# Performance work log

Measured on AMD Instinct MI355X. Metric: run time of the kernel, lower is better.

## Reference

```python
import jax, jax.numpy as jnp
import numpy as np

B, C, H, W = 16, 256, 96, 96
CQ = C // 8      # 32, query/key channels in CrossAttention
CM = C // 2      # 128, inter_planes


def conv1x1(x, w, b=None):
    # x: [B,Cin,H,W], w: [Cout,Cin]
    y = jnp.einsum('bchw,oc->bohw', x, w)
    if b is not None:
        y = y + b[None, :, None, None]
    return y


def cross_attention(x, wq, bq, wk, bk, wv, bv, gamma):
    # criss-cross (axial H and W) attention with -inf diagonal on the H branch
    b_, c_, h_, w_ = x.shape
    q = conv1x1(x, wq, bq)  # [B,CQ,H,W]
    k = conv1x1(x, wk, bk)
    v = conv1x1(x, wv, bv)  # [B,C,H,W]
    # energy over column (H axis): [B,H,W,H], masked diag h==h'
    e_h = jnp.einsum('bchw,bckw->bhwk', q, k)
    diag = jnp.eye(h_, dtype=bool)[None, :, None, :]  # [1,H,1,H]
    e_h = jnp.where(diag, -jnp.inf, e_h)
    # energy over row (W axis): [B,H,W,W]
    e_w = jnp.einsum('bchw,bchv->bhwv', q, k)
    att = jax.nn.softmax(jnp.concatenate([e_h, e_w], axis=3), axis=3)
    a_h, a_w = att[..., :h_], att[..., h_:]
    out_h = jnp.einsum('bckw,bhwk->bchw', v, a_h)
    out_w = jnp.einsum('bchv,bhwv->bchw', v, a_w)
    return gamma * (out_h + out_w) + x


def spatial_weighted(x, w_q_right, w_v_right, w_up, b_up):
    b_, _, h_, w_ = x.shape
    inp = conv1x1(x, w_v_right).reshape(b_, CM, h_ * w_)        # [B,CM,HW]
    mask = conv1x1(x, w_q_right).reshape(b_, 1, h_ * w_)        # [B,1,HW]
    mask = jax.nn.softmax(mask, axis=2)
    ctx = jnp.einsum('bcn,bon->bco', inp, mask)                 # [B,CM,1]
    ctx = jnp.einsum('bci,oc->boi', ctx, w_up) + b_up[None, :, None]  # [B,C,1]
    mask_ch = jax.nn.sigmoid(ctx)[..., None]                    # [B,C,1,1]
    return x * mask_ch


def channel_weighted(x, w_q_left, w_v_left):
    b_, _, h_, w_ = x.shape
    g = conv1x1(x, w_q_left)                                    # [B,CM,H,W]
    avg = jnp.mean(g, axis=(2, 3))                              # [B,CM]
    theta = conv1x1(x, w_v_left).reshape(b_, CM, h_ * w_)       # [B,CM,HW]
    ctx = jnp.einsum('bc,bcn->bn', avg, theta)                  # [B,HW]
    ctx = jax.nn.softmax(ctx, axis=1).reshape(b_, 1, h_, w_)
    return x * jax.nn.sigmoid(ctx)


def setup_inputs() -> dict:
    key = jax.random.key(0)
    ks = jax.random.split(key, 16)
    s = lambda fan_in: (2.0 / fan_in) ** 0.5
    inp = {
        'x': jax.random.normal(ks[0], (B, C, H, W), jnp.float32),
        'w_q_right': jax.random.normal(ks[1], (1, C), jnp.float32) * s(C),
        'w_v_right': jax.random.normal(ks[2], (CM, C), jnp.float32) * s(C),
        'w_up': jax.random.normal(ks[3], (C, CM), jnp.float32) * s(CM),
        'b_up': jnp.zeros((C,), jnp.float32),
        'w_q_left': jax.random.normal(ks[4], (CM, C), jnp.float32) * s(C),
        'w_v_left': jax.random.normal(ks[5], (CM, C), jnp.float32) * s(C),
        'cr_wq': jax.random.normal(ks[6], (CQ, C), jnp.float32) * s(C),
        'cr_bq': jnp.zeros((CQ,), jnp.float32),
        'cr_wk': jax.random.normal(ks[7], (CQ, C), jnp.float32) * s(C),
        'cr_bk': jnp.zeros((CQ,), jnp.float32),
        'cr_wv': jax.random.normal(ks[8], (C, C), jnp.float32) * s(C),
        'cr_bv': jnp.zeros((C,), jnp.float32),
        'gamma': jax.random.normal(ks[9], (1,), jnp.float32) * 0.1,
    }
    return inp


def reference(x, w_q_right, w_v_right, w_up, b_up, w_q_left, w_v_left,
              cr_wq, cr_bq, cr_wk, cr_bk, cr_wv, cr_bv, gamma):
    cross = lambda t: cross_attention(t, cr_wq, cr_bq, cr_wk, cr_bk, cr_wv, cr_bv, gamma)
    ctx_channel = cross(spatial_weighted(x, w_q_right, w_v_right, w_up, b_up))
    ctx_spatial = cross(channel_weighted(x, w_q_left, w_v_left))
    return cross(ctx_spatial + ctx_channel)
```

## Files before the change

### kernel.cpp

```cpp
#include <hip/hip_runtime.h>
#include <math.h>

#define Bn 16
#define Cn 256
#define CQn 32
#define CMn 128
#define Hn 96
#define Wn 96
#define Nn 9216
#define PIXn 147456

typedef short bf8 __attribute__((ext_vector_type(8)));
typedef float f32x4 __attribute__((ext_vector_type(4)));
#define MFMA(a,b,c) __builtin_amdgcn_mfma_f32_16x16x32_bf16(a,b,c,0,0,0)

typedef unsigned short ushort_t;

__device__ inline ushort_t f2bf(float f){
  union{float f; unsigned int u;} v; v.f=f;
  unsigned int r = v.u + 0x7fffu + ((v.u>>16)&1u);
  return (ushort_t)(r>>16);
}
__device__ inline float bf2f(ushort_t s){
  union{unsigned int u; float f;} v; v.u = ((unsigned int)s)<<16;
  return v.f;
}

__device__ inline float waveSum(float v){
#pragma unroll
  for(int o=32;o;o>>=1) v += __shfl_down(v,o,64);
  return v;
}
__device__ inline float waveMax(float v){
#pragma unroll
  for(int o=32;o;o>>=1) v = fmaxf(v,__shfl_down(v,o,64));
  return v;
}


__global__ __launch_bounds__(1024) void k_pass1(const float* __restrict__ x,
    const float* __restrict__ wqr, float* __restrict__ xmean,
    float* __restrict__ partp){
  int cg = blockIdx.x, b = blockIdx.y, tid = threadIdx.x;
  __shared__ float r16[16];
  float mp[9];
#pragma unroll
  for(int k=0;k<9;k++) mp[k]=0.f;
  for(int cc=0;cc<16;cc++){
    int c = cg*16+cc;
    const float* row = x + ((size_t)b*Cn + c)*Nn;
    float w = wqr[c];
    float s = 0.f;
#pragma unroll
    for(int k=0;k<9;k++){
      float v = row[k*1024+tid];
      s += v;
      mp[k] += w*v;
    }
    s = waveSum(s);
    if((tid&63)==0) r16[tid>>6]=s;
    __syncthreads();
    if(tid==0){
      float t=0.f;
      for(int i=0;i<16;i++) t+=r16[i];
      xmean[(size_t)b*Cn + c] = t*(1.f/Nn);
    }
    __syncthreads();
  }
  float* dst = partp + ((size_t)cg*Bn + b)*Nn;
#pragma unroll
  for(int k=0;k<9;k++) dst[k*1024+tid]=mp[k];
}

__global__ __launch_bounds__(1024) void k_pass2(const float* __restrict__ x,
    const float* __restrict__ wvec, const float* __restrict__ maskb,
    float* __restrict__ xw, float* __restrict__ partp){
  int cg = blockIdx.x, b = blockIdx.y, tid = threadIdx.x;
  __shared__ float r16[16];
  float cp[9], mk[9];
#pragma unroll
  for(int k=0;k<9;k++){
    cp[k]=0.f;
    mk[k]=maskb[(size_t)b*Nn + k*1024+tid];
  }
  for(int cc=0;cc<16;cc++){
    int c = cg*16+cc;
    const float* row = x + ((size_t)b*Cn + c)*Nn;
    float w = wvec[(size_t)b*Cn + c];
    float s = 0.f;
#pragma unroll
    for(int k=0;k<9;k++){
      float v = row[k*1024+tid];
      s += mk[k]*v;
      cp[k] += w*v;
    }
    s = waveSum(s);
    if((tid&63)==0) r16[tid>>6]=s;
    __syncthreads();
    if(tid==0){
      float t=0.f;
      for(int i=0;i<16;i++) t+=r16[i];
      xw[(size_t)b*Cn + c] = t;
    }
    __syncthreads();
  }
  float* dst = partp + ((size_t)cg*Bn + b)*Nn;
#pragma unroll
  for(int k=0;k<9;k++) dst[k*1024+tid]=cp[k];
}

__global__ void k_red16(const float* __restrict__ part, float* __restrict__ out){
  size_t p = (size_t)blockIdx.x*256 + threadIdx.x;
  float s=0.f;
#pragma unroll
  for(int cg=0;cg<16;cg++) s += part[(size_t)cg*Bn*Nn + p];
  out[p]=s;
}

__global__ void k_small1(const float* __restrict__ xmean, const float* __restrict__ wql,
                         const float* __restrict__ wvl, float* __restrict__ wvec){
  int b=blockIdx.x, t=threadIdx.x;
  __shared__ float xm[Cn];
  __shared__ float av[CMn];
  xm[t] = xmean[b*Cn+t];
  __syncthreads();
  if(t<CMn){
    float s=0.f;
    for(int c=0;c<Cn;c++) s += wql[t*Cn+c]*xm[c];
    av[t]=s;
  }
  __syncthreads();
  float s=0.f;
  for(int m=0;m<CMn;m++) s += av[m]*wvl[m*Cn+t];
  wvec[b*Cn+t]=s;
}

__global__ void k_softmax_n(const float* __restrict__ in, float* __restrict__ out, int mode){
  int b=blockIdx.x, tid=threadIdx.x, lane=tid&63, wid=tid>>6;
  const float* p = in + (size_t)b*Nn;
  __shared__ float red[16];
  __shared__ float bc2[2];
  float mx=-3e38f;
  for(int i=tid;i<Nn;i+=1024) mx=fmaxf(mx,p[i]);
  mx = waveMax(mx);
  if(lane==0) red[wid]=mx;
  __syncthreads();
  if(tid==0){ float m=red[0]; for(int i=1;i<16;i++) m=fmaxf(m,red[i]); bc2[0]=m; }
  __syncthreads();
  mx=bc2[0];
  float s=0.f;
  for(int i=tid;i<Nn;i+=1024) s+=expf(p[i]-mx);
  s = waveSum(s);
  __syncthreads();
  if(lane==0) red[wid]=s;
  __syncthreads();
  if(tid==0){ float t=0.f; for(int i=0;i<16;i++) t+=red[i]; bc2[1]=t; }
  __syncthreads();
  float inv=1.f/bc2[1];
  for(int i=tid;i<Nn;i+=1024){
    float e=expf(p[i]-mx)*inv;
    out[(size_t)b*Nn+i] = mode ? 1.f/(1.f+expf(-e)) : e;
  }
}

__global__ void k_small2(const float* __restrict__ xw, const float* __restrict__ wvr,
                         const float* __restrict__ wup, const float* __restrict__ bup,
                         float* __restrict__ g1){
  int b=blockIdx.x, t=threadIdx.x;
  __shared__ float xs[Cn];
  __shared__ float cx[CMn];
  xs[t]=xw[b*Cn+t];
  __syncthreads();
  if(t<CMn){
    float s=0.f;
    for(int c=0;c<Cn;c++) s += wvr[t*Cn+c]*xs[c];
    cx[t]=s;
  }
  __syncthreads();
  float s=bup[t];
  for(int m=0;m<CMn;m++) s += wup[t*CMn+m]*cx[m];
  g1[b*Cn+t]=1.f/(1.f+expf(-s));
}

__global__ void k_gates(const float* __restrict__ x, const float* __restrict__ g1,
                        const float* __restrict__ m2, ushort_t* __restrict__ t1,
                        ushort_t* __restrict__ t2){
  size_t i4 = ((size_t)blockIdx.x*256 + threadIdx.x)*4;
  int n  = (int)(i4 % Nn);
  int bc = (int)(i4 / Nn);
  int b  = bc / Cn;
  float4 xv = *(const float4*)&x[i4];
  float g = g1[bc];
  float4 mv = *(const float4*)&m2[(size_t)b*Nn + n];
  uint2 a, c;
  a.x = (unsigned)f2bf(xv.x*g) | ((unsigned)f2bf(xv.y*g)<<16);
  a.y = (unsigned)f2bf(xv.z*g) | ((unsigned)f2bf(xv.w*g)<<16);
  c.x = (unsigned)f2bf(xv.x*mv.x) | ((unsigned)f2bf(xv.y*mv.y)<<16);
  c.y = (unsigned)f2bf(xv.z*mv.z) | ((unsigned)f2bf(xv.w*mv.w)<<16);
  *(uint2*)&t1[i4] = a;
  *(uint2*)&t2[i4] = c;
}


__global__ void k_packb(const float* __restrict__ wq, const float* __restrict__ bq,
                        const float* __restrict__ wk, const float* __restrict__ bk,
                        const float* __restrict__ wv, const float* __restrict__ bv,
                        ushort_t* __restrict__ Wp, float* __restrict__ bp){
  int o = blockIdx.x, t = threadIdx.x;
  const float* src; float bs;
  if(o<32){ src = wq + o*Cn; bs = bq[o]; }
  else if(o<64){ src = wk + (o-32)*Cn; bs = bk[o-32]; }
  else { src = wv + (o-64)*Cn; bs = bv[o-64]; }
  Wp[o*Cn+t] = f2bf(src[t]);
  if(t==0) bp[o] = bs;
}

#define AP 40
#define BP 264

__global__ __launch_bounds__(256) void k_gemm_qkv(const ushort_t* __restrict__ x,
    const ushort_t* __restrict__ Wp, const float* __restrict__ bp,
    ushort_t* __restrict__ Yqk, ushort_t* __restrict__ Vb){
  __shared__ ushort_t Ws[320*AP];
  __shared__ ushort_t Bt[64*BP];
  int b  = blockIdx.y;
  int n0 = blockIdx.x*64;
  int tid = threadIdx.x, lane = tid&63, wid = tid>>6;

  {
    const ushort_t* xb = x + (size_t)b*Cn*Nn + n0 + (tid&63);
    int cg = (tid>>6)*8;
#pragma unroll
    for(int p=0;p<8;p++){
      int c8 = p*32 + cg;
      unsigned e0=xb[(size_t)(c8+0)*Nn], e1=xb[(size_t)(c8+1)*Nn];
      unsigned e2=xb[(size_t)(c8+2)*Nn], e3=xb[(size_t)(c8+3)*Nn];
      unsigned e4=xb[(size_t)(c8+4)*Nn], e5=xb[(size_t)(c8+5)*Nn];
      unsigned e6=xb[(size_t)(c8+6)*Nn], e7=xb[(size_t)(c8+7)*Nn];
      uint4 pk;
      pk.x = e0 | (e1<<16); pk.y = e2 | (e3<<16);
      pk.z = e4 | (e5<<16); pk.w = e6 | (e7<<16);
      *(uint4*)&Bt[(tid&63)*BP + c8] = pk;
    }
  }

  f32x4 acc[5][4];
#pragma unroll
  for(int f=0;f<5;f++)
#pragma unroll
    for(int g=0;g<4;g++) acc[f][g] = (f32x4){0.f,0.f,0.f,0.f};

  for(int ki=0;ki<8;ki++){
    __syncthreads();
#pragma unroll
    for(int q=0;q<5;q++){
      int fidx = q*256 + tid;
      int o = fidx>>2, kk = (fidx&3)*8;
      uint4 wv = *(const uint4*)&Wp[o*Cn + ki*32 + kk];
      *(uint4*)&Ws[o*AP + kk] = wv;
    }
    __syncthreads();
    bf8 bfr[4];
#pragma unroll
    for(int g=0;g<4;g++)
      bfr[g] = *(const bf8*)&Bt[(g*16 + (lane&15))*BP + ki*32 + (lane>>4)*8];
#pragma unroll
    for(int f=0;f<5;f++){
      bf8 a = *(const bf8*)&Ws[(wid*80 + f*16 + (lane&15))*AP + (lane>>4)*8];
#pragma unroll
      for(int g=0;g<4;g++) acc[f][g] = MFMA(a, bfr[g], acc[f][g]);
    }
  }

#pragma unroll
  for(int f=0;f<5;f++){
    int ob = wid*80 + f*16 + (lane>>4)*4;
#pragma unroll
    for(int i=0;i<4;i++){
      int o = ob + i;
      float bias = bp[o];
      ushort_t* dst = (o<64) ? (Yqk + ((size_t)b*64 + o)*Nn)
                             : (Vb + ((size_t)b*Cn + (o-64))*Nn);
#pragma unroll
      for(int g=0;g<4;g++)
        dst[n0 + g*16 + (lane&15)] = f2bf(acc[f][g][i] + bias);
    }
  }
}

__global__ __launch_bounds__(256) void k_transpose_b(const ushort_t* __restrict__ src,
                                                     ushort_t* __restrict__ dst){
  __shared__ ushort_t Ls[96*98];
  size_t base = (size_t)blockIdx.x * Nn;
  int tid = threadIdx.x;
  for(int e=tid*2; e<Nn; e+=512){
    unsigned int u = *(const unsigned int*)&src[base+e];
    int r=e/96, c=e%96;
    *(unsigned int*)&Ls[r*98+c] = u;
  }
  __syncthreads();
  for(int e=tid*2; e<Nn; e+=512){
    int r=e/96, c=e%96;
    unsigned int u = (unsigned int)Ls[c*98+r] | (((unsigned int)Ls[(c+1)*98+r])<<16);
    *(unsigned int*)&dst[base+e] = u;
  }
}

__global__ __launch_bounds__(256) void k_e2(const ushort_t* __restrict__ Yqk,
    const ushort_t* __restrict__ Yqkt, float* __restrict__ att){
  __shared__ ushort_t Qt[96*AP];
  __shared__ ushort_t Kt[96*AP];
  int r = blockIdx.x, mode = blockIdx.y, b = blockIdx.z;
  const ushort_t* Y = mode ? Yqk : Yqkt;
  int aoff = mode ? 96 : 0;
  int pm   = mode ? 1  : 96;
  int pr   = mode ? 96 : 1;
  int tid = threadIdx.x, lane = tid&63, wid = tid>>6;
  {
    int half = tid>>7;
    int cg   = (tid>>5)&3;
    int l32  = tid&31;
    ushort_t* T = half ? Kt : Qt;
    const ushort_t* S = Y + ((size_t)b*64 + half*32 + cg*8)*Nn + (size_t)r*96;
#pragma unroll
    for(int p=0;p<3;p++){
      int sp = p*32 + l32;
      unsigned e0=S[(size_t)0*Nn+sp], e1=S[(size_t)1*Nn+sp];
      unsigned e2=S[(size_t)2*Nn+sp], e3=S[(size_t)3*Nn+sp];
      unsigned e4=S[(size_t)4*Nn+sp], e5=S[(size_t)5*Nn+sp];
      unsigned e6=S[(size_t)6*Nn+sp], e7=S[(size_t)7*Nn+sp];
      uint4 pk;
      pk.x = e0 | (e1<<16); pk.y = e2 | (e3<<16);
      pk.z = e4 | (e5<<16); pk.w = e6 | (e7<<16);
      *(uint4*)&T[sp*AP + cg*8] = pk;
    }
  }
  __syncthreads();
  int mb = (wid>>1)*48, nb = (wid&1)*48;
  const f32x4 z4 = {0.f,0.f,0.f,0.f};
  f32x4 acc[3][3];
  bf8 a[3], bb[3];
#pragma unroll
  for(int f=0;f<3;f++) a[f] = *(const bf8*)&Qt[(mb+f*16+(lane&15))*AP + (lane>>4)*8];
#pragma unroll
  for(int g=0;g<3;g++) bb[g] = *(const bf8*)&Kt[(nb+g*16+(lane&15))*AP + (lane>>4)*8];
#pragma unroll
  for(int f=0;f<3;f++)
#pragma unroll
    for(int g=0;g<3;g++) acc[f][g] = MFMA(a[f], bb[g], z4);
  int diag = (mode==0);
#pragma unroll
  for(int f=0;f<3;f++)
#pragma unroll
    for(int i=0;i<4;i++){
      int m = mb + f*16 + (lane>>4)*4 + i;
      float* arow = att + ((size_t)b*Nn + (size_t)m*pm + (size_t)r*pr)*192 + aoff;
#pragma unroll
      for(int g=0;g<3;g++){
        int n = nb + g*16 + (lane&15);
        arow[n] = (diag && n==m) ? -1e30f : acc[f][g][i];
      }
    }
}

__global__ void k_softmax_att(const float* __restrict__ att,
    ushort_t* __restrict__ attw, ushort_t* __restrict__ atth){
  int wave = threadIdx.x>>6, lane = threadIdx.x&63;
  int p = blockIdx.x*4 + wave;
  const float* a = att + (size_t)p*192;
  float v0=a[lane], v1=a[lane+64], v2=a[lane+128];
  float mx = fmaxf(v0, fmaxf(v1,v2));
#pragma unroll
  for(int o=32;o;o>>=1) mx = fmaxf(mx, __shfl_xor(mx,o,64));
  float e0=expf(v0-mx), e1=expf(v1-mx), e2=expf(v2-mx);
  float s=e0+e1+e2;
#pragma unroll
  for(int o=32;o;o>>=1) s += __shfl_xor(s,o,64);
  float inv=1.f/s;
  int b = p/Nn, rem = p%Nn, h = rem/96, w = rem%96;
  ushort_t* ph = atth + ((size_t)b*Nn + (size_t)w*96 + h)*96;
  ushort_t* pw = attw + (size_t)p*96;
  ph[lane] = f2bf(e0*inv);
  if(lane<32) ph[64+lane] = f2bf(e1*inv);
  else        pw[lane-32] = f2bf(e1*inv);
  pw[lane+32] = f2bf(e2*inv);
}

#define SP 120

template<int OUTF>
__global__ __launch_bounds__(512) void k_pv2(const ushort_t* __restrict__ Vb,
    const ushort_t* __restrict__ VT, const ushort_t* __restrict__ attw,
    const ushort_t* __restrict__ atth, const ushort_t* resid,
    float* __restrict__ Of, ushort_t* OwB, ushort_t* OT,
    const float* __restrict__ gp){
  __shared__ ushort_t As[96*SP];
  int r = blockIdx.x, mode = blockIdx.y, b = blockIdx.z;
  float gm = gp[0];
  int tid = threadIdx.x, lane = tid&63, wid = tid>>6;
  const ushort_t* V = mode ? VT : Vb;
  size_t vbase = (size_t)b*Cn*Nn + (size_t)r*96;
  bf8 vf[6];
#pragma unroll
  for(int f=0;f<2;f++)
#pragma unroll
    for(int j=0;j<3;j++)
      vf[f*3+j] = *(const bf8*)&V[vbase
        + (size_t)(wid*32 + f*16 + (lane&15))*Nn + j*32 + (lane>>4)*8];
  const ushort_t* ab = (mode ? atth : attw) + ((size_t)b*Nn + (size_t)r*96)*96;
  for(int u=tid; u<96*12; u+=512){
    int n=u/12, j8=(u%12)*8;
    uint4 q = *(const uint4*)&ab[n*96 + j8];
    *(uint4*)&As[n*SP + j8] = q;
  }
  __syncthreads();
  f32x4 acc[2][6];
#pragma unroll
  for(int f=0;f<2;f++)
#pragma unroll
    for(int g=0;g<6;g++) acc[f][g] = (f32x4){0.f,0.f,0.f,0.f};
#pragma unroll
  for(int j0=0;j0<3;j0++){
    bf8 bfr[6];
#pragma unroll
    for(int g=0;g<6;g++)
      bfr[g] = *(const bf8*)&As[(g*16+(lane&15))*SP + j0*32 + (lane>>4)*8];
#pragma unroll
    for(int f=0;f<2;f++)
#pragma unroll
      for(int g=0;g<6;g++) acc[f][g] = MFMA(vf[f*3+j0], bfr[g], acc[f][g]);
  }
#pragma unroll
  for(int f=0;f<2;f++){
    int cb = wid*32 + f*16 + (lane>>4)*4;
#pragma unroll
    for(int i=0;i<4;i++){
      size_t row = vbase + (size_t)(cb+i)*Nn;
      if(mode){
#pragma unroll
        for(int g=0;g<6;g++){
          int n = g*16 + (lane&15);
          OT[row+n] = f2bf(gm*acc[f][g][i]);
        }
      } else {
#pragma unroll
        for(int g=0;g<6;g++){
          int n = g*16 + (lane&15);
          float val = gm*acc[f][g][i] + bf2f(resid[row+n]);
          if(OUTF) Of[row+n] = val;
          else     OwB[row+n] = f2bf(val);
        }
      }
    }
  }
}

template<int VAR>
__global__ __launch_bounds__(256) void k_merge(float* __restrict__ outf,
    ushort_t* __restrict__ outb, const ushort_t* __restrict__ add,
    const ushort_t* __restrict__ OT){
  __shared__ ushort_t Ls[96*98];
  size_t base = (size_t)blockIdx.x * Nn;
  int tid = threadIdx.x;
  for(int e=tid*2; e<Nn; e+=512){
    unsigned int u = *(const unsigned int*)&OT[base+e];
    int r=e/96, c=e%96;
    *(unsigned int*)&Ls[r*98+c] = u;
  }
  __syncthreads();
  for(int e=tid*4; e<Nn; e+=1024){
    int r=e/96, c=e%96;
    float t0 = bf2f(Ls[(c+0)*98+r]), t1 = bf2f(Ls[(c+1)*98+r]);
    float t2 = bf2f(Ls[(c+2)*98+r]), t3 = bf2f(Ls[(c+3)*98+r]);
    if(VAR==1){
      float4 o = *(float4*)&outf[base+e];
      o.x += t0; o.y += t1; o.z += t2; o.w += t3;
      *(float4*)&outf[base+e] = o;
    } else {
      uint2 u = *(uint2*)&outb[base+e];
      float a0 = bf2f((ushort_t)(u.x&0xffff)) + t0;
      float a1 = bf2f((ushort_t)(u.x>>16))    + t1;
      float a2 = bf2f((ushort_t)(u.y&0xffff)) + t2;
      float a3 = bf2f((ushort_t)(u.y>>16))    + t3;
      if(VAR==2){
        uint2 v = *(const uint2*)&add[base+e];
        a0 += bf2f((ushort_t)(v.x&0xffff));
        a1 += bf2f((ushort_t)(v.x>>16));
        a2 += bf2f((ushort_t)(v.y&0xffff));
        a3 += bf2f((ushort_t)(v.y>>16));
      }
      u.x = (unsigned)f2bf(a0) | ((unsigned)f2bf(a1)<<16);
      u.y = (unsigned)f2bf(a2) | ((unsigned)f2bf(a3)<<16);
      *(uint2*)&outb[base+e] = u;
    }
  }
}

extern "C" void kernel_launch(void* const* d_in, const int* in_sizes, int n_in,
                              void* d_out, int out_size, void* d_ws, size_t ws_size,
                              hipStream_t stream){
  const float* x    = (const float*)d_in[0];
  const float* wqr  = (const float*)d_in[1];
  const float* wvr  = (const float*)d_in[2];
  const float* wup  = (const float*)d_in[3];
  const float* bup  = (const float*)d_in[4];
  const float* wql  = (const float*)d_in[5];
  const float* wvl  = (const float*)d_in[6];
  const float* crwq = (const float*)d_in[7];
  const float* crbq = (const float*)d_in[8];
  const float* crwk = (const float*)d_in[9];
  const float* crbk = (const float*)d_in[10];
  const float* crwv = (const float*)d_in[11];
  const float* crbv = (const float*)d_in[12];
  const float* gma  = (const float*)d_in[13];
  float* out = (float*)d_out;

  const size_t XSZ = (size_t)Bn*Cn*Nn;
  const size_t YSZ = (size_t)Bn*64*Nn;
  char* wsb = (char*)d_ws;
  ushort_t* T1   = (ushort_t*)wsb; wsb += XSZ*2;
  ushort_t* T2   = (ushort_t*)wsb; wsb += XSZ*2;
  ushort_t* Vb   = (ushort_t*)wsb; wsb += XSZ*2;
  ushort_t* Yqk  = (ushort_t*)wsb; wsb += YSZ*2;
  ushort_t* Yqkt = (ushort_t*)wsb; wsb += YSZ*2;
  float*    ATT  = (float*)wsb;    wsb += (size_t)PIXn*192*4;
  ushort_t* VT   = (ushort_t*)ATT;
  ushort_t* ATTw = (ushort_t*)wsb; wsb += (size_t)PIXn*96*2;
  ushort_t* ATTh = (ushort_t*)wsb; wsb += (size_t)PIXn*96*2;
  float*    partp= (float*)wsb;    wsb += (size_t)16*Bn*Nn*4;
  ushort_t* Wpb  = (ushort_t*)wsb; wsb += 320*Cn*2;
  float*    bp   = (float*)wsb;    wsb += 320*4;
  float*    xmean= (float*)wsb;    wsb += Bn*Cn*4;
  float*    wvec = (float*)wsb;    wsb += Bn*Cn*4;
  float*    xw   = (float*)wsb;    wsb += Bn*Cn*4;
  float*    g1   = (float*)wsb;    wsb += Bn*Cn*4;
  float*    mraw = (float*)wsb;    wsb += (size_t)PIXn*4;
  float*    maskb= (float*)wsb;    wsb += (size_t)PIXn*4;
  float*    craw = (float*)wsb;    wsb += (size_t)PIXn*4;
  float*    m2   = (float*)wsb;    wsb += (size_t)PIXn*4;

  k_packb<<<320,256,0,stream>>>(crwq,crbq,crwk,crbk,crwv,crbv,Wpb,bp);

  k_pass1<<<dim3(16,Bn),1024,0,stream>>>(x, wqr, xmean, partp);
  k_red16<<<Bn*Nn/256,256,0,stream>>>(partp, mraw);
  k_small1<<<Bn,256,0,stream>>>(xmean, wql, wvl, wvec);
  k_softmax_n<<<Bn,1024,0,stream>>>(mraw, maskb, 0);
  k_pass2<<<dim3(16,Bn),1024,0,stream>>>(x, wvec, maskb, xw, partp);
  k_red16<<<Bn*Nn/256,256,0,stream>>>(partp, craw);
  k_softmax_n<<<Bn,1024,0,stream>>>(craw, m2, 1);
  k_small2<<<Bn,256,0,stream>>>(xw, wvr, wup, bup, g1);
  k_gates<<<XSZ/1024,256,0,stream>>>(x, g1, m2, T1, T2);

  auto cross = [&](const ushort_t* t, ushort_t* ob, float* of, int var){
    k_gemm_qkv<<<dim3(Nn/64,Bn),256,0,stream>>>(t, Wpb, bp, Yqk, Vb);
    k_transpose_b<<<Bn*64,256,0,stream>>>(Yqk, Yqkt);
    k_e2<<<dim3(96,2,Bn),256,0,stream>>>(Yqk, Yqkt, ATT);
    k_softmax_att<<<PIXn/4,256,0,stream>>>(ATT, ATTw, ATTh);
    k_transpose_b<<<Bn*Cn,256,0,stream>>>(Vb, VT);
    if(var==1) k_pv2<1><<<dim3(96,2,Bn),512,0,stream>>>(Vb, VT, ATTw, ATTh, t, of, nullptr, VT, gma);
    else       k_pv2<0><<<dim3(96,2,Bn),512,0,stream>>>(Vb, VT, ATTw, ATTh, t, nullptr, ob, VT, gma);
    if(var==0)      k_merge<0><<<Bn*Cn,256,0,stream>>>(nullptr, ob, nullptr, VT);
    else if(var==1) k_merge<1><<<Bn*Cn,256,0,stream>>>(of, nullptr, nullptr, VT);
    else            k_merge<2><<<Bn*Cn,256,0,stream>>>(nullptr, T1, T2, VT);
  };

  cross(T1, T1, nullptr, 0);
  cross(T2, T2, nullptr, 2);
  cross(T1, nullptr, out, 1);
}
```

Before: 1.222 ms.

## Store attention energies as fp16 and stage GEMM/PV outputs through LDS for vector stores

Attention energies are now written as fp16 into two separate 96-wide buffers instead of a 192-wide fp32 buffer. The diagonal mask moves into the softmax kernel. The QKV GEMM and PV kernels stage their outputs through shared memory so that global writes (and residual reads) become coalesced 16-byte vector accesses instead of scattered 2-byte stores. VT gets its own buffer rather than aliasing ATT. The intent is to cut memory traffic and store inefficiency, at the cost of extra syncs and reduced energy precision.

```diff
diff --git a/kernel.cpp b/kernel.cpp
--- a/kernel.cpp
+++ b/kernel.cpp
@@ -15,6 +15,7 @@
 #define MFMA(a,b,c) __builtin_amdgcn_mfma_f32_16x16x32_bf16(a,b,c,0,0,0)
 
 typedef unsigned short ushort_t;
+typedef _Float16 h16;
 
 __device__ inline ushort_t f2bf(float f){
   union{float f; unsigned int u;} v; v.f=f;
@@ -24,6 +25,12 @@
 __device__ inline float bf2f(ushort_t s){
   union{unsigned int u; float f;} v; v.u = ((unsigned int)s)<<16;
   return v.f;
+}
+__device__ inline ushort_t f2h(float f){
+  union{h16 h; ushort_t u;} v; v.h=(h16)f; return v.u;
+}
+__device__ inline float h2f(ushort_t u){
+  union{ushort_t u; h16 h;} v; v.u=u; return (float)v.h;
 }
 
 __device__ inline float waveSum(float v){
@@ -217,6 +224,7 @@
 
 #define AP 40
 #define BP 264
+#define GP 68
 
 __global__ __launch_bounds__(256) void k_gemm_qkv(const ushort_t* __restrict__ x,
     const ushort_t* __restrict__ Wp, const float* __restrict__ bp,
@@ -272,18 +280,28 @@
     }
   }
 
-#pragma unroll
-  for(int f=0;f<5;f++){
-    int ob = wid*80 + f*16 + (lane>>4)*4;
-#pragma unroll
-    for(int i=0;i<4;i++){
-      int o = ob + i;
-      float bias = bp[o];
+  for(int q=0;q<4;q++){
+    __syncthreads();
+    if(wid==q){
+#pragma unroll
+      for(int f=0;f<5;f++){
+        int lr = f*16 + (lane>>4)*4;
+#pragma unroll
+        for(int i=0;i<4;i++){
+          float bias = bp[q*80 + lr + i];
+#pragma unroll
+          for(int g=0;g<4;g++)
+            Ws[(lr+i)*GP + g*16 + (lane&15)] = f2bf(acc[f][g][i] + bias);
+        }
+      }
+    }
+    __syncthreads();
+    for(int u=tid; u<80*8; u+=256){
+      int lo_ = u>>3, c8 = (u&7)*8;
+      int o = q*80 + lo_;
       ushort_t* dst = (o<64) ? (Yqk + ((size_t)b*64 + o)*Nn)
                              : (Vb + ((size_t)b*Cn + (o-64))*Nn);
-#pragma unroll
-      for(int g=0;g<4;g++)
-        dst[n0 + g*16 + (lane&15)] = f2bf(acc[f][g][i] + bias);
+      *(uint4*)&dst[n0 + c8] = *(uint4*)&Ws[lo_*GP + c8];
     }
   }
 }
@@ -307,14 +325,15 @@
 }
 
 __global__ __launch_bounds__(256) void k_e2(const ushort_t* __restrict__ Yqk,
-    const ushort_t* __restrict__ Yqkt, float* __restrict__ att){
+    const ushort_t* __restrict__ Yqkt, ushort_t* __restrict__ attl,
+    ushort_t* __restrict__ attr){
   __shared__ ushort_t Qt[96*AP];
   __shared__ ushort_t Kt[96*AP];
   int r = blockIdx.x, mode = blockIdx.y, b = blockIdx.z;
   const ushort_t* Y = mode ? Yqk : Yqkt;
-  int aoff = mode ? 96 : 0;
   int pm   = mode ? 1  : 96;
   int pr   = mode ? 96 : 1;
+  ushort_t* attx = mode ? attr : attl;
   int tid = threadIdx.x, lane = tid&63, wid = tid>>6;
   {
     int half = tid>>7;
@@ -348,27 +367,38 @@
   for(int f=0;f<3;f++)
 #pragma unroll
     for(int g=0;g<3;g++) acc[f][g] = MFMA(a[f], bb[g], z4);
-  int diag = (mode==0);
 #pragma unroll
   for(int f=0;f<3;f++)
 #pragma unroll
     for(int i=0;i<4;i++){
       int m = mb + f*16 + (lane>>4)*4 + i;
-      float* arow = att + ((size_t)b*Nn + (size_t)m*pm + (size_t)r*pr)*192 + aoff;
+      ushort_t* arow = attx + ((size_t)b*Nn + (size_t)m*pm + (size_t)r*pr)*96;
 #pragma unroll
       for(int g=0;g<3;g++){
         int n = nb + g*16 + (lane&15);
-        arow[n] = (diag && n==m) ? -1e30f : acc[f][g][i];
+        arow[n] = f2h(acc[f][g][i]);
       }
     }
 }
 
-__global__ void k_softmax_att(const float* __restrict__ att,
+__global__ void k_softmax_att(const ushort_t* __restrict__ attl,
+    const ushort_t* __restrict__ attr,
     ushort_t* __restrict__ attw, ushort_t* __restrict__ atth){
   int wave = threadIdx.x>>6, lane = threadIdx.x&63;
   int p = blockIdx.x*4 + wave;
-  const float* a = att + (size_t)p*192;
-  float v0=a[lane], v1=a[lane+64], v2=a[lane+128];
+  const ushort_t* al = attl + (size_t)p*96;
+  const ushort_t* ar = attr + (size_t)p*96;
+  int b = p/Nn, rem = p%Nn, h = rem/96, w = rem%96;
+  float v0 = h2f(al[lane]);
+  if(lane==h) v0 = -1e30f;
+  float v1;
+  if(lane<32){
+    v1 = h2f(al[64+lane]);
+    if(64+lane==h) v1 = -1e30f;
+  } else {
+    v1 = h2f(ar[lane-32]);
+  }
+  float v2 = h2f(ar[lane+32]);
   float mx = fmaxf(v0, fmaxf(v1,v2));
 #pragma unroll
   for(int o=32;o;o>>=1) mx = fmaxf(mx, __shfl_xor(mx,o,64));
@@ -377,7 +407,6 @@
 #pragma unroll
   for(int o=32;o;o>>=1) s += __shfl_xor(s,o,64);
   float inv=1.f/s;
-  int b = p/Nn, rem = p%Nn, h = rem/96, w = rem%96;
   ushort_t* ph = atth + ((size_t)b*Nn + (size_t)w*96 + h)*96;
   ushort_t* pw = attw + (size_t)p*96;
   ph[lane] = f2bf(e0*inv);
@@ -387,6 +416,7 @@
 }
 
 #define SP 120
+#define RP 100
 
 template<int OUTF>
 __global__ __launch_bounds__(512) void k_pv2(const ushort_t* __restrict__ Vb,
@@ -394,7 +424,7 @@
     const ushort_t* __restrict__ atth, const ushort_t* resid,
     float* __restrict__ Of, ushort_t* OwB, ushort_t* OT,
     const float* __restrict__ gp){
-  __shared__ ushort_t As[96*SP];
+  __shared__ ushort_t SMEM[128*RP];
   int r = blockIdx.x, mode = blockIdx.y, b = blockIdx.z;
   float gm = gp[0];
   int tid = threadIdx.x, lane = tid&63, wid = tid>>6;
@@ -411,7 +441,7 @@
   for(int u=tid; u<96*12; u+=512){
     int n=u/12, j8=(u%12)*8;
     uint4 q = *(const uint4*)&ab[n*96 + j8];
-    *(uint4*)&As[n*SP + j8] = q;
+    *(uint4*)&SMEM[n*SP + j8] = q;
   }
   __syncthreads();
   f32x4 acc[2][6];
@@ -424,31 +454,57 @@
     bf8 bfr[6];
 #pragma unroll
     for(int g=0;g<6;g++)
-      bfr[g] = *(const bf8*)&As[(g*16+(lane&15))*SP + j0*32 + (lane>>4)*8];
+      bfr[g] = *(const bf8*)&SMEM[(g*16+(lane&15))*SP + j0*32 + (lane>>4)*8];
 #pragma unroll
     for(int f=0;f<2;f++)
 #pragma unroll
       for(int g=0;g<6;g++) acc[f][g] = MFMA(vf[f*3+j0], bfr[g], acc[f][g]);
   }
-#pragma unroll
-  for(int f=0;f<2;f++){
-    int cb = wid*32 + f*16 + (lane>>4)*4;
-#pragma unroll
-    for(int i=0;i<4;i++){
-      size_t row = vbase + (size_t)(cb+i)*Nn;
+  for(int half=0; half<2; half++){
+    __syncthreads();
+    if((wid>>2)==half){
+#pragma unroll
+      for(int f=0;f<2;f++){
+        int lr = (wid&3)*32 + f*16 + (lane>>4)*4;
+#pragma unroll
+        for(int i=0;i<4;i++)
+#pragma unroll
+          for(int g=0;g<6;g++)
+            SMEM[(lr+i)*RP + g*16 + (lane&15)] = f2bf(gm*acc[f][g][i]);
+      }
+    }
+    __syncthreads();
+    for(int u=tid; u<128*12; u+=512){
+      int lc = u/12, q8 = (u%12)*8;
+      size_t row = vbase + (size_t)(half*128 + lc)*Nn;
+      uint4 v = *(uint4*)&SMEM[lc*RP + q8];
       if(mode){
-#pragma unroll
-        for(int g=0;g<6;g++){
-          int n = g*16 + (lane&15);
-          OT[row+n] = f2bf(gm*acc[f][g][i]);
-        }
+        *(uint4*)&OT[row + q8] = v;
       } else {
-#pragma unroll
-        for(int g=0;g<6;g++){
-          int n = g*16 + (lane&15);
-          float val = gm*acc[f][g][i] + bf2f(resid[row+n]);
-          if(OUTF) Of[row+n] = val;
-          else     OwB[row+n] = f2bf(val);
+        uint4 rv = *(const uint4*)&resid[row + q8];
+        unsigned* vp=(unsigned*)&v; unsigned* rp=(unsigned*)&rv;
+        if(OUTF){
+          float4 o1, o2;
+          o1.x = bf2f((ushort_t)(vp[0]&0xffff)) + bf2f((ushort_t)(rp[0]&0xffff));
+          o1.y = bf2f((ushort_t)(vp[0]>>16))    + bf2f((ushort_t)(rp[0]>>16));
+          o1.z = bf2f((ushort_t)(vp[1]&0xffff)) + bf2f((ushort_t)(rp[1]&0xffff));
+          o1.w = bf2f((ushort_t)(vp[1]>>16))    + bf2f((ushort_t)(rp[1]>>16));
+          o2.x = bf2f((ushort_t)(vp[2]&0xffff)) + bf2f((ushort_t)(rp[2]&0xffff));
+          o2.y = bf2f((ushort_t)(vp[2]>>16))    + bf2f((ushort_t)(rp[2]>>16));
+          o2.z = bf2f((ushort_t)(vp[3]&0xffff)) + bf2f((ushort_t)(rp[3]&0xffff));
+          o2.w = bf2f((ushort_t)(vp[3]>>16))    + bf2f((ushort_t)(rp[3]>>16));
+          *(float4*)&Of[row + q8]     = o1;
+          *(float4*)&Of[row + q8 + 4] = o2;
+        } else {
+          uint4 o;
+          unsigned* op=(unsigned*)&o;
+#pragma unroll
+          for(int k=0;k<4;k++){
+            float lo = bf2f((ushort_t)(vp[k]&0xffff)) + bf2f((ushort_t)(rp[k]&0xffff));
+            float hi = bf2f((ushort_t)(vp[k]>>16))    + bf2f((ushort_t)(rp[k]>>16));
+            op[k] = (unsigned)f2bf(lo) | ((unsigned)f2bf(hi)<<16);
+          }
+          *(uint4*)&OwB[row + q8] = o;
         }
       }
     }
@@ -521,10 +577,11 @@
   ushort_t* T1   = (ushort_t*)wsb; wsb += XSZ*2;
   ushort_t* T2   = (ushort_t*)wsb; wsb += XSZ*2;
   ushort_t* Vb   = (ushort_t*)wsb; wsb += XSZ*2;
+  ushort_t* VT   = (ushort_t*)wsb; wsb += XSZ*2;
   ushort_t* Yqk  = (ushort_t*)wsb; wsb += YSZ*2;
   ushort_t* Yqkt = (ushort_t*)wsb; wsb += YSZ*2;
-  float*    ATT  = (float*)wsb;    wsb += (size_t)PIXn*192*4;
-  ushort_t* VT   = (ushort_t*)ATT;
+  ushort_t* ATTL = (ushort_t*)wsb; wsb += (size_t)PIXn*96*2;
+  ushort_t* ATTR = (ushort_t*)wsb; wsb += (size_t)PIXn*96*2;
   ushort_t* ATTw = (ushort_t*)wsb; wsb += (size_t)PIXn*96*2;
   ushort_t* ATTh = (ushort_t*)wsb; wsb += (size_t)PIXn*96*2;
   float*    partp= (float*)wsb;    wsb += (size_t)16*Bn*Nn*4;
@@ -554,8 +611,8 @@
   auto cross = [&](const ushort_t* t, ushort_t* ob, float* of, int var){
     k_gemm_qkv<<<dim3(Nn/64,Bn),256,0,stream>>>(t, Wpb, bp, Yqk, Vb);
     k_transpose_b<<<Bn*64,256,0,stream>>>(Yqk, Yqkt);
-    k_e2<<<dim3(96,2,Bn),256,0,stream>>>(Yqk, Yqkt, ATT);
-    k_softmax_att<<<PIXn/4,256,0,stream>>>(ATT, ATTw, ATTh);
+    k_e2<<<dim3(96,2,Bn),256,0,stream>>>(Yqk, Yqkt, ATTL, ATTR);
+    k_softmax_att<<<PIXn/4,256,0,stream>>>(ATTL, ATTR, ATTw, ATTh);
     k_transpose_b<<<Bn*Cn,256,0,stream>>>(Vb, VT);
     if(var==1) k_pv2<1><<<dim3(96,2,Bn),512,0,stream>>>(Vb, VT, ATTw, ATTh, t, of, nullptr, VT, gma);
     else       k_pv2<0><<<dim3(96,2,Bn),512,0,stream>>>(Vb, VT, ATTw, ATTh, t, nullptr, ob, VT, gma);
```

After: 1.243 ms. About the same (+1.8%).
